# Kernel optimization log

Measured on AMD Instinct MI355X. Metric: run time of the kernel, lower is better.

## Reference

```python
import jax, jax.numpy as jnp
import numpy as np

WEIGHT = 100.0
ALPHA = 20.0
MAX_ITER = 1000
STOP_THR = 0.005
EPS = 1e-16
CHECK_EVERY = 50  # torch code checks convergence every 50 iters


def setup_inputs() -> dict:
    key = jax.random.key(0)
    T, V = 512, 32000
    cost = jax.random.uniform(key, (T, V), dtype=jnp.float32)
    return {"cost": cost}


def reference(cost):
    T, V = cost.shape
    a = jnp.full((T, 1), 1.0 / T, dtype=cost.dtype)
    b = jnp.full((V, 1), 1.0 / V, dtype=cost.dtype)
    K = jnp.exp(-ALPHA * cost)  # [T, V]

    def sinkhorn_step(carry, _):
        u, v = carry
        v = b / (K.T @ u + EPS)  # [V, 1]
        u = a / (K @ v + EPS)    # [T, 1]
        return (u, v), None

    # while_loop over chunks of CHECK_EVERY iterations, with the same
    # every-50-iters convergence check as the torch loop.
    def cond(state):
        it, u, v, err = state
        return (it < MAX_ITER) & (err >= STOP_THR)

    def body(state):
        it, u, v, err = state
        (u, v), _ = jax.lax.scan(sinkhorn_step, (u, v), None, length=CHECK_EVERY)
        err = jnp.abs(v * (K.T @ u) - b).sum()
        return (it + CHECK_EVERY, u, v, err)

    init = (jnp.int32(0), a, jnp.zeros((V, 1), cost.dtype), jnp.array(jnp.inf, cost.dtype))
    _, u, v, _ = jax.lax.while_loop(cond, body, init)

    pi = u * (K * v.T)  # [T, V] transport plan
    return WEIGHT * (pi * cost).sum()
```

## Files before the change

### kernel.cpp

```cpp
#include <hip/hip_runtime.h>
#include <math.h>

#define TT 512
#define VV 32000
#define NB 250
#define NTHR 512
#define BCOLS 128
#define MAXIT 1000
#define CHK 50
#define NCHK (MAXIT / CHK)
#define LDS_BYTES 136576

typedef float f4 __attribute__((ext_vector_type(4)));
typedef _Float16 h8 __attribute__((ext_vector_type(8)));
typedef _Float16 h2 __attribute__((ext_vector_type(2)));
typedef unsigned long long u64;

template <int CTRL>
__device__ __forceinline__ float dpp_add(float x) {
  int y = __builtin_amdgcn_update_dpp(0, __builtin_bit_cast(int, x), CTRL, 0xF, 0xF, true);
  return x + __builtin_bit_cast(float, y);
}
__device__ __forceinline__ float red16(float x) {
  x = dpp_add<0x111>(x); x = dpp_add<0x112>(x);
  x = dpp_add<0x114>(x); x = dpp_add<0x118>(x);
  return x;
}
__device__ __forceinline__ float red32(float x) {
  x = red16(x); x = dpp_add<0x142>(x); return x;
}
__device__ __forceinline__ float red64(float x) {
  x = red32(x); x = dpp_add<0x143>(x); return x;
}

__device__ __forceinline__ int fswz(int row) { return (row ^ (row >> 5)) & 15; }

__device__ __forceinline__ u64 ald(const u64* p) {
  return __hip_atomic_load((const u64*)p, __ATOMIC_RELAXED, __HIP_MEMORY_SCOPE_AGENT);
}
__device__ __forceinline__ void ast(u64* p, u64 v) {
  __hip_atomic_store(p, v, __ATOMIC_RELAXED, __HIP_MEMORY_SCOPE_AGENT);
}

extern "C" __global__ void __launch_bounds__(NTHR, 1)
sink_kernel(const float* __restrict__ cost, u64* __restrict__ partial,
            u64* __restrict__ upair, float* __restrict__ errb,
            float* __restrict__ lossp) {
  extern __shared__ char smem[];
  h8*       tile8  = (h8*)smem;
  float*    uf     = (float*)(smem + 131072);
  float*    u_prev = (float*)(smem + 133120);
  float*    vf     = (float*)(smem + 135168);
  float*    v_prev = (float*)(smem + 135680);
  _Float16* vh     = (_Float16*)(smem + 136192);
  h8*       vh8    = (h8*)vh;
  float*    errw   = (float*)(smem + 136448);
  float*    wred   = (float*)(smem + 136512);

  const int t  = threadIdx.x;
  const int b  = blockIdx.x;
  const int cB = t & 15;
  const int rB = t >> 4;
  const int gA = t >> 5;
  const int sA = t & 31;

  const float* cb = cost + (size_t)b * BCOLS;

  for (int i = 0; i < 16; ++i) {
    int row = rB + 32 * i;
    const float* p = cb + (size_t)row * VV + cB * 8;
    f4 x0 = *(const f4*)p;
    f4 x1 = *(const f4*)(p + 4);
    h8 kk;
#pragma unroll
    for (int e = 0; e < 4; ++e) kk[e]     = (_Float16)__expf(-20.f * x0[e]);
#pragma unroll
    for (int e = 0; e < 4; ++e) kk[4 + e] = (_Float16)__expf(-20.f * x1[e]);
    tile8[row * 16 + (cB ^ fswz(row))] = kk;
  }
  uf[t] = 1.0f;
  __syncthreads();

  const bool writerA = ((t & 31) == 31);
  const int rlo = (b * TT) / NB, rhi = ((b + 1) * TT) / NB;
  const int wv = t >> 6, ln = t & 63;
  bool converged = false;

  for (int it = 0; it < MAXIT; ++it) {
    const bool chk = (it > 0) && (it % CHK == 0);
    const int ci = it / CHK - 1;
    const unsigned st = (unsigned)(it + 1);
    const u64 stamp = ((u64)st) << 32;

    float acc[8];
#pragma unroll
    for (int e = 0; e < 8; ++e) acc[e] = 0.f;
    f4 u4[4];
#pragma unroll
    for (int k = 0; k < 4; ++k) u4[k] = ((const f4*)uf)[sA * 4 + k];
#pragma unroll
    for (int i = 0; i < 16; ++i) {
      int row = sA * 16 + i;
      h8 kk = tile8[row * 16 + (gA ^ fswz(row))];
      float uu = u4[i >> 2][i & 3];
#pragma unroll
      for (int e = 0; e < 8; ++e) acc[e] = fmaf((float)kk[e], uu, acc[e]);
    }
#pragma unroll
    for (int e = 0; e < 8; ++e) acc[e] = red32(acc[e]);

    if (chk) u_prev[t] = uf[t];

    if (writerA) {
      float el = 0.f;
#pragma unroll
      for (int e = 0; e < 8; ++e) {
        float sa = acc[e] * (1.f / TT);
        float vo = vf[gA * 8 + e];
        if (chk) { el += fabsf(vo * sa - 1.f); v_prev[gA * 8 + e] = vo; }
        float nv = 1.f / (sa + 1e-16f);
        vf[gA * 8 + e] = nv;
        vh[gA * 8 + e] = (_Float16)nv;
      }
      if (chk) errw[gA] = el;
    }
    __syncthreads();
    if (chk) {
      if (t == 0) {
        float s = 0.f;
#pragma unroll
        for (int w = 0; w < 16; ++w) s += errw[w];
        __hip_atomic_fetch_add(&errb[ci], s, __ATOMIC_RELAXED, __HIP_MEMORY_SCOPE_AGENT);
      }
      __syncthreads();
    }

    h8 vv = vh8[cB];
#pragma unroll
    for (int i = 0; i < 16; ++i) {
      int row = rB + 32 * i;
      h8 kk = tile8[row * 16 + (cB ^ fswz(row))];
      float rs = 0.f;
      rs = __builtin_amdgcn_fdot2(h2{kk[0], kk[1]}, h2{vv[0], vv[1]}, rs, false);
      rs = __builtin_amdgcn_fdot2(h2{kk[2], kk[3]}, h2{vv[2], vv[3]}, rs, false);
      rs = __builtin_amdgcn_fdot2(h2{kk[4], kk[5]}, h2{vv[4], vv[5]}, rs, false);
      rs = __builtin_amdgcn_fdot2(h2{kk[6], kk[7]}, h2{vv[6], vv[7]}, rs, false);
      rs = red16(rs);
      if ((t & 15) == 15)
        ast(&partial[(size_t)b * TT + row], stamp | (u64)__builtin_bit_cast(unsigned, rs));
    }

    if (wv < rhi - rlo) {
      int row = rlo + wv;
      float vals[4];
      for (;;) {
        bool done = true;
#pragma unroll
        for (int k = 0; k < 4; ++k) {
          int bb = ln + 64 * k;
          vals[k] = 0.f;
          if (bb < NB) {
            u64 pv = ald(&partial[(size_t)bb * TT + row]);
            done = done && ((unsigned)(pv >> 32) == st);
            vals[k] = __builtin_bit_cast(float, (unsigned)pv);
          }
        }
        if (__all(done)) break;
        __builtin_amdgcn_s_sleep(1);
      }
      float s = vals[0] + vals[1] + vals[2] + vals[3];
      s = red64(s);
      if (ln == 63) {
        float unew = 1.f / (s * (1.f / VV) + 1e-16f);
        ast(&upair[row], stamp | (u64)__builtin_bit_cast(unsigned, unew));
      }
    }

    {
      u64 pv;
      for (;;) {
        pv = ald(&upair[t]);
        if ((unsigned)(pv >> 32) == st) break;
        __builtin_amdgcn_s_sleep(1);
      }
      uf[t] = __builtin_bit_cast(float, (unsigned)pv);
    }
    __syncthreads();

    if (chk) {
      if (t == 0) wred[0] = __hip_atomic_load(&errb[ci], __ATOMIC_RELAXED, __HIP_MEMORY_SCOPE_AGENT);
      __syncthreads();
      if (wred[0] < 0.005f * VV) { converged = true; break; }
    }
  }

  if (converged) {
    uf[t] = u_prev[t];
    if (t < 128) vf[t] = v_prev[t];
    __syncthreads();
  }

  float lacc = 0.f;
  for (int i = 0; i < 16; ++i) {
    int row = rB + 32 * i;
    const float* p = cb + (size_t)row * VV + cB * 8;
    f4 x0 = *(const f4*)p;
    f4 x1 = *(const f4*)(p + 4);
    float um = uf[row];
    float inner = 0.f;
#pragma unroll
    for (int e = 0; e < 4; ++e) inner = fmaf(vf[cB * 8 + e] * __expf(-20.f * x0[e]), x0[e], inner);
#pragma unroll
    for (int e = 0; e < 4; ++e) inner = fmaf(vf[cB * 8 + 4 + e] * __expf(-20.f * x1[e]), x1[e], inner);
    lacc = fmaf(um, inner, lacc);
  }
  lacc = red64(lacc);
  if ((t & 63) == 63) wred[t >> 6] = lacc;
  __syncthreads();
  if (t == 0) {
    float s = 0.f;
#pragma unroll
    for (int w = 0; w < 8; ++w) s += wred[w];
    lossp[b] = s;
  }
}

extern "C" __global__ void prep_kernel(u64* zbuf, int nz, float* errb, float* out) {
  int gid = threadIdx.x + blockIdx.x * 256;
  for (int i = gid; i < nz; i += gridDim.x * 256) zbuf[i] = 0ull;
  if (gid < NCHK) errb[gid] = 0.f;
  if (gid == 0) out[0] = 0.f;
}

extern "C" __global__ void final_kernel(const float* __restrict__ lossp, float* __restrict__ out) {
  int t = threadIdx.x;
  float s = 0.f;
  for (int i = t; i < NB; i += 64) s += lossp[i];
  s = red64(s);
  if (t == 63) out[0] = s * (100.0f / ((float)TT * (float)VV));
}

extern "C" void kernel_launch(void* const* d_in, const int* in_sizes, int n_in,
                              void* d_out, int out_size, void* d_ws, size_t ws_size,
                              hipStream_t stream) {
  const float* cost = (const float*)d_in[0];
  float* out = (float*)d_out;
  char* ws = (char*)d_ws;
  u64*   partial = (u64*)ws;
  u64*   upair   = (u64*)(ws + 1048576);
  float* errb    = (float*)(ws + 1052672);
  float* lossp   = (float*)(ws + 1052800);

  const int nz = 250 * TT + TT;
  prep_kernel<<<512, 256, 0, stream>>>(partial, nz, errb, out);

  (void)hipFuncSetAttribute((const void*)sink_kernel,
                            hipFuncAttributeMaxDynamicSharedMemorySize, LDS_BYTES);
  void* args[] = {(void*)&cost, (void*)&partial, (void*)&upair, (void*)&errb, (void*)&lossp};
  (void)hipLaunchCooperativeKernel((const void*)sink_kernel, dim3(NB), dim3(NTHR),
                                   args, LDS_BYTES, stream);

  final_kernel<<<1, 64, 0, stream>>>(lossp, out);
}
```

Baseline: 659.7 us.

## Pipeline u-gather into K^T u pass and fuse row reduction into partial loop

Removes the end-of-iteration barrier where all threads polled upair. Instead, wave 0 polls upair in 64-row chunks and publishes per-chunk LDS flags, so the other waves can start the K^T u accumulation as soon as each chunk arrives. The owner reduction of partials now runs inside the K v loop at the chunk that contains the owned row, which overlaps it with the remaining partial writes. The convergence test is deferred by one iteration so it overlaps with useful work. In exchange it adds intra-workgroup spin-waits on LDS flags, drops the s_sleep backoff, and loosens unrolling, which risks contention and more complex ordering.

```diff
diff --git a/kernel.cpp b/kernel.cpp
--- a/kernel.cpp
+++ b/kernel.cpp
@@ -36,10 +36,13 @@
 __device__ __forceinline__ int fswz(int row) { return (row ^ (row >> 5)) & 15; }
 
 __device__ __forceinline__ u64 ald(const u64* p) {
-  return __hip_atomic_load((const u64*)p, __ATOMIC_RELAXED, __HIP_MEMORY_SCOPE_AGENT);
+  return __hip_atomic_load(p, __ATOMIC_RELAXED, __HIP_MEMORY_SCOPE_AGENT);
 }
 __device__ __forceinline__ void ast(u64* p, u64 v) {
   __hip_atomic_store(p, v, __ATOMIC_RELAXED, __HIP_MEMORY_SCOPE_AGENT);
+}
+__device__ __forceinline__ float aldf(const float* p) {
+  return __hip_atomic_load(p, __ATOMIC_RELAXED, __HIP_MEMORY_SCOPE_AGENT);
 }
 
 extern "C" __global__ void __launch_bounds__(NTHR, 1)
@@ -56,6 +59,7 @@
   h8*       vh8    = (h8*)vh;
   float*    errw   = (float*)(smem + 136448);
   float*    wred   = (float*)(smem + 136512);
+  int*      jflag  = (int*)(smem + 136544);
 
   const int t  = threadIdx.x;
   const int b  = blockIdx.x;
@@ -63,6 +67,7 @@
   const int rB = t >> 4;
   const int gA = t >> 5;
   const int sA = t & 31;
+  const int wv = t >> 6, ln = t & 63;
 
   const float* cb = cost + (size_t)b * BCOLS;
 
@@ -78,38 +83,75 @@
     for (int e = 0; e < 4; ++e) kk[4 + e] = (_Float16)__expf(-20.f * x1[e]);
     tile8[row * 16 + (cB ^ fswz(row))] = kk;
   }
-  uf[t] = 1.0f;
+  if (t < 8) jflag[t] = 0;
   __syncthreads();
 
+  const int rlo = (b * TT) / NB, rhi = ((b + 1) * TT) / NB;
   const bool writerA = ((t & 31) == 31);
-  const int rlo = (b * TT) / NB, rhi = ((b + 1) * TT) / NB;
-  const int wv = t >> 6, ln = t & 63;
   bool converged = false;
 
   for (int it = 0; it < MAXIT; ++it) {
-    const bool chk = (it > 0) && (it % CHK == 0);
-    const int ci = it / CHK - 1;
-    const unsigned st = (unsigned)(it + 1);
-    const u64 stamp = ((u64)st) << 32;
+    const unsigned stU = (unsigned)(it + 1);
+    const u64 pstamp  = ((u64)(it + 1)) << 32;
+    const u64 ustampP = ((u64)(it + 2)) << 32;
+    const bool chkc = (it > 0) && (it % CHK == 0);
+    const bool pending = ((it % CHK) == 1) && (it > CHK);
+    const int ciW = it / CHK - 1;
+    const int ciR = (it - 1) / CHK - 1;
+
+    if (pending) { u_prev[t] = uf[t]; __syncthreads(); }
 
     float acc[8];
 #pragma unroll
     for (int e = 0; e < 8; ++e) acc[e] = 0.f;
-    f4 u4[4];
-#pragma unroll
-    for (int k = 0; k < 4; ++k) u4[k] = ((const f4*)uf)[sA * 4 + k];
-#pragma unroll
-    for (int i = 0; i < 16; ++i) {
-      int row = sA * 16 + i;
-      h8 kk = tile8[row * 16 + (gA ^ fswz(row))];
-      float uu = u4[i >> 2][i & 3];
-#pragma unroll
-      for (int e = 0; e < 8; ++e) acc[e] = fmaf((float)kk[e], uu, acc[e]);
-    }
+
+    if (t < 64) {
+#pragma unroll 1
+      for (int j = 0; j < 8; ++j) {
+        u64 pv;
+        for (;;) {
+          pv = ald(&upair[64 * j + t]);
+          if (__all((unsigned)(pv >> 32) == stU)) break;
+        }
+        uf[64 * j + t] = __builtin_bit_cast(float, (unsigned)pv);
+        asm volatile("s_waitcnt lgkmcnt(0)" ::: "memory");
+        if (t == 0)
+          __hip_atomic_store(&jflag[j], (int)stU, __ATOMIC_RELEASE,
+                             __HIP_MEMORY_SCOPE_WORKGROUP);
+        if (pending && j == 0) {
+          if (aldf(&errb[ciR]) < 0.005f * VV) { converged = true; break; }
+        }
+#pragma unroll
+        for (int ii = 0; ii < 2; ++ii) {
+          int row = 64 * j + 32 * ii + sA;
+          h8 kk = tile8[row * 16 + (gA ^ fswz(row))];
+          float uu = uf[row];
+#pragma unroll
+          for (int e = 0; e < 8; ++e) acc[e] = fmaf((float)kk[e], uu, acc[e]);
+        }
+      }
+    } else {
+#pragma unroll 1
+      for (int j = 0; j < 8; ++j) {
+        while (__hip_atomic_load(&jflag[j], __ATOMIC_ACQUIRE,
+                                 __HIP_MEMORY_SCOPE_WORKGROUP) != (int)stU) {}
+        if (pending && j == 0) {
+          if (aldf(&errb[ciR]) < 0.005f * VV) { converged = true; break; }
+        }
+#pragma unroll
+        for (int ii = 0; ii < 2; ++ii) {
+          int row = 64 * j + 32 * ii + sA;
+          h8 kk = tile8[row * 16 + (gA ^ fswz(row))];
+          float uu = uf[row];
+#pragma unroll
+          for (int e = 0; e < 8; ++e) acc[e] = fmaf((float)kk[e], uu, acc[e]);
+        }
+      }
+    }
+    if (converged) break;
+
 #pragma unroll
     for (int e = 0; e < 8; ++e) acc[e] = red32(acc[e]);
-
-    if (chk) u_prev[t] = uf[t];
 
     if (writerA) {
       float el = 0.f;
@@ -117,26 +159,29 @@
       for (int e = 0; e < 8; ++e) {
         float sa = acc[e] * (1.f / TT);
         float vo = vf[gA * 8 + e];
-        if (chk) { el += fabsf(vo * sa - 1.f); v_prev[gA * 8 + e] = vo; }
+        if (chkc) { el += fabsf(vo * sa - 1.f); v_prev[gA * 8 + e] = vo; }
         float nv = 1.f / (sa + 1e-16f);
         vf[gA * 8 + e] = nv;
         vh[gA * 8 + e] = (_Float16)nv;
       }
-      if (chk) errw[gA] = el;
+      if (chkc) errw[gA] = el;
     }
     __syncthreads();
-    if (chk) {
+    if (chkc) {
       if (t == 0) {
         float s = 0.f;
 #pragma unroll
         for (int w = 0; w < 16; ++w) s += errw[w];
-        __hip_atomic_fetch_add(&errb[ci], s, __ATOMIC_RELAXED, __HIP_MEMORY_SCOPE_AGENT);
+        __hip_atomic_fetch_add(&errb[ciW], s, __ATOMIC_RELAXED, __HIP_MEMORY_SCOPE_AGENT);
       }
       __syncthreads();
     }
 
     h8 vv = vh8[cB];
-#pragma unroll
+    const bool isowner = (wv < rhi - rlo);
+    const int orow = rlo + wv;
+    const int ochunk = orow >> 5;
+#pragma unroll 1
     for (int i = 0; i < 16; ++i) {
       int row = rB + 32 * i;
       h8 kk = tile8[row * 16 + (cB ^ fswz(row))];
@@ -147,56 +192,47 @@
       rs = __builtin_amdgcn_fdot2(h2{kk[6], kk[7]}, h2{vv[6], vv[7]}, rs, false);
       rs = red16(rs);
       if ((t & 15) == 15)
-        ast(&partial[(size_t)b * TT + row], stamp | (u64)__builtin_bit_cast(unsigned, rs));
-    }
-
-    if (wv < rhi - rlo) {
-      int row = rlo + wv;
-      float vals[4];
-      for (;;) {
-        bool done = true;
-#pragma unroll
-        for (int k = 0; k < 4; ++k) {
-          int bb = ln + 64 * k;
-          vals[k] = 0.f;
-          if (bb < NB) {
-            u64 pv = ald(&partial[(size_t)bb * TT + row]);
-            done = done && ((unsigned)(pv >> 32) == st);
-            vals[k] = __builtin_bit_cast(float, (unsigned)pv);
+        ast(&partial[(size_t)b * TT + row], pstamp | (u64)__builtin_bit_cast(unsigned, rs));
+      if (isowner && i == ochunk) {
+        float vals[4];
+        for (;;) {
+          bool done = true;
+#pragma unroll
+          for (int k = 0; k < 4; ++k) {
+            int bb = ln + 64 * k;
+            vals[k] = 0.f;
+            if (bb < NB) {
+              u64 pvv = ald(&partial[(size_t)bb * TT + orow]);
+              done = done && ((unsigned)(pvv >> 32) == stU);
+              vals[k] = __builtin_bit_cast(float, (unsigned)pvv);
+            }
           }
-        }
-        if (__all(done)) break;
-        __builtin_amdgcn_s_sleep(1);
-      }
-      float s = vals[0] + vals[1] + vals[2] + vals[3];
-      s = red64(s);
-      if (ln == 63) {
-        float unew = 1.f / (s * (1.f / VV) + 1e-16f);
-        ast(&upair[row], stamp | (u64)__builtin_bit_cast(unsigned, unew));
-      }
-    }
-
-    {
-      u64 pv;
-      for (;;) {
-        pv = ald(&upair[t]);
-        if ((unsigned)(pv >> 32) == st) break;
-        __builtin_amdgcn_s_sleep(1);
-      }
-      uf[t] = __builtin_bit_cast(float, (unsigned)pv);
-    }
+          if (__all(done)) break;
+        }
+        float s = vals[0] + vals[1] + vals[2] + vals[3];
+        s = red64(s);
+        if (ln == 63) {
+          float unew = 1.f / (s * (1.f / VV) + 1e-16f);
+          ast(&upair[orow], ustampP | (u64)__builtin_bit_cast(unsigned, unew));
+        }
+      }
+    }
+  }
+
+  if (converged) {
     __syncthreads();
-
-    if (chk) {
-      if (t == 0) wred[0] = __hip_atomic_load(&errb[ci], __ATOMIC_RELAXED, __HIP_MEMORY_SCOPE_AGENT);
-      __syncthreads();
-      if (wred[0] < 0.005f * VV) { converged = true; break; }
-    }
-  }
-
-  if (converged) {
     uf[t] = u_prev[t];
     if (t < 128) vf[t] = v_prev[t];
+    __syncthreads();
+  } else {
+    if (t < 64) {
+#pragma unroll 1
+      for (int j = 0; j < 8; ++j) {
+        u64 pvv;
+        do { pvv = ald(&upair[64 * j + t]); } while ((unsigned)(pvv >> 32) != (unsigned)(MAXIT + 1));
+        uf[64 * j + t] = __builtin_bit_cast(float, (unsigned)pvv);
+      }
+    }
     __syncthreads();
   }
 
@@ -225,9 +261,10 @@
   }
 }
 
-extern "C" __global__ void prep_kernel(u64* zbuf, int nz, float* errb, float* out) {
+extern "C" __global__ void prep_kernel(u64* partial, u64* upair, float* errb, float* out) {
   int gid = threadIdx.x + blockIdx.x * 256;
-  for (int i = gid; i < nz; i += gridDim.x * 256) zbuf[i] = 0ull;
+  for (int i = gid; i < NB * TT; i += gridDim.x * 256) partial[i] = 0ull;
+  if (gid < TT) upair[gid] = (1ull << 32) | (u64)0x3f800000u;
   if (gid < NCHK) errb[gid] = 0.f;
   if (gid == 0) out[0] = 0.f;
 }
@@ -251,8 +288,7 @@
   float* errb    = (float*)(ws + 1052672);
   float* lossp   = (float*)(ws + 1052800);
 
-  const int nz = 250 * TT + TT;
-  prep_kernel<<<512, 256, 0, stream>>>(partial, nz, errb, out);
+  prep_kernel<<<512, 256, 0, stream>>>(partial, upair, errb, out);
 
   (void)hipFuncSetAttribute((const void*)sink_kernel,
                             hipFuncAttributeMaxDynamicSharedMemorySize, LDS_BYTES);
```

New measurement: 1.689 ms. 156% more time.
